# Performance work log

Hardware: AMD Instinct MI355X
Metric: run time of the kernel (lower is better)

## Reference

```python
import jax, jax.numpy as jnp
import numpy as np

EPS_COS = 1e-8   # torch CosineSimilarity default eps
EP = 0.001       # module's self.ep


def _cosine_sim(a, b):
    # torch.nn.CosineSimilarity(dim=1): dot / max(||a||*||b||, eps)
    dot = jnp.sum(a * b, axis=1)
    na = jnp.sqrt(jnp.sum(a * a, axis=1))
    nb = jnp.sqrt(jnp.sum(b * b, axis=1))
    return dot / jnp.maximum(na * nb, EPS_COS)


def setup_inputs() -> dict:
    key = jax.random.key(0)
    k1, k2, k3, k4 = jax.random.split(key, 4)
    B, D = 4096, 1024
    return {
        "question_embeddings_pos": jax.random.normal(k1, (2 * B, D), dtype=jnp.float32),
        "question_embeddings_neg": jax.random.normal(k2, (23 * B, D), dtype=jnp.float32),
        "pos_image_embeddings": jax.random.normal(k3, (2 * B, D), dtype=jnp.float32),
        "neg_image_embeddings": jax.random.normal(k4, (23 * B, D), dtype=jnp.float32),
        "batch_size": B,
    }


def reference(question_embeddings_pos, question_embeddings_neg,
              pos_image_embeddings, neg_image_embeddings, batch_size):
    epos = jnp.exp(_cosine_sim(question_embeddings_pos, pos_image_embeddings))  # [2B]
    eneg = jnp.exp(_cosine_sim(question_embeddings_neg, neg_image_embeddings))  # [23B]
    # segmented sums: groups of 2 positives and 23 negatives per batch item
    pos_sum = jnp.sum(epos.reshape(batch_size, 2), axis=1)    # [B]
    neg_sum = jnp.sum(eneg.reshape(batch_size, 23), axis=1)   # [B]
    per_item = (neg_sum - pos_sum) / (pos_sum + neg_sum + EP)
    return jnp.sum(per_item)
```

## Files before the change

### kernel.cpp

```cpp
#include <hip/hip_runtime.h>
#include <math.h>

#define D 1024
#define EPS_COS 1e-8f
#define EP 0.001f

__global__ __launch_bounds__(256) void row_cosexp_kernel(
    const float* __restrict__ qpos, const float* __restrict__ ipos,
    const float* __restrict__ qneg, const float* __restrict__ ineg,
    float* __restrict__ e, int n_pos, int n_total)
{
    const int row  = (int)((blockIdx.x * blockDim.x + threadIdx.x) >> 6);
    const int lane = threadIdx.x & 63;
    if (row >= n_total) return;

    const float* a;
    const float* b;
    if (row < n_pos) {
        a = qpos + (size_t)row * D;
        b = ipos + (size_t)row * D;
    } else {
        const size_t rn = (size_t)(row - n_pos);
        a = qneg + rn * D;
        b = ineg + rn * D;
    }
    const float4* a4 = (const float4*)a;
    const float4* b4 = (const float4*)b;

    float dab = 0.f, daa = 0.f, dbb = 0.f;
#pragma unroll
    for (int j = 0; j < 4; ++j) {
        const float4 av = a4[lane + 64 * j];
        const float4 bv = b4[lane + 64 * j];
        dab += av.x * bv.x + av.y * bv.y + av.z * bv.z + av.w * bv.w;
        daa += av.x * av.x + av.y * av.y + av.z * av.z + av.w * av.w;
        dbb += bv.x * bv.x + bv.y * bv.y + bv.z * bv.z + bv.w * bv.w;
    }

#pragma unroll
    for (int off = 32; off > 0; off >>= 1) {
        dab += __shfl_down(dab, off, 64);
        daa += __shfl_down(daa, off, 64);
        dbb += __shfl_down(dbb, off, 64);
    }

    if (lane == 0) {
        const float denom = fmaxf(sqrtf(daa) * sqrtf(dbb), EPS_COS);
        e[row] = __expf(dab / denom);
    }
}

__global__ __launch_bounds__(256) void combine_kernel(
    const float* __restrict__ e, float* __restrict__ out, int B, int n_pos)
{
    const int i = (int)(blockIdx.x * blockDim.x + threadIdx.x);
    float v = 0.f;
    if (i < B) {
        const float ps = e[2 * i] + e[2 * i + 1];
        const float* en = e + n_pos + 23 * (size_t)i;
        float ns = 0.f;
#pragma unroll
        for (int j = 0; j < 23; ++j) ns += en[j];
        v = (ns - ps) / (ps + ns + EP);
    }

#pragma unroll
    for (int off = 32; off > 0; off >>= 1) v += __shfl_down(v, off, 64);

    __shared__ float s[4];
    const int lane = threadIdx.x & 63;
    const int w    = threadIdx.x >> 6;
    if (lane == 0) s[w] = v;
    __syncthreads();
    if (threadIdx.x == 0) {
        const float t = s[0] + s[1] + s[2] + s[3];
        atomicAdd(out, t);
    }
}

extern "C" void kernel_launch(void* const* d_in, const int* in_sizes, int n_in,
                              void* d_out, int out_size, void* d_ws, size_t ws_size,
                              hipStream_t stream) {
    const float* qpos = (const float*)d_in[0];
    const float* qneg = (const float*)d_in[1];
    const float* ipos = (const float*)d_in[2];
    const float* ineg = (const float*)d_in[3];

    const int B       = in_sizes[0] / (2 * D);
    const int n_pos   = 2 * B;
    const int n_neg   = 23 * B;
    const int n_total = n_pos + n_neg;

    float* e = (float*)d_ws;

    hipMemsetAsync(d_out, 0, sizeof(float), stream);

    const int rows_per_block = 256 / 64;
    const int grid1 = (n_total + rows_per_block - 1) / rows_per_block;
    row_cosexp_kernel<<<grid1, 256, 0, stream>>>(qpos, ipos, qneg, ineg, e, n_pos, n_total);

    const int grid2 = (B + 255) / 256;
    combine_kernel<<<grid2, 256, 0, stream>>>(e, (float*)d_out, B, n_pos);
}
```

Baseline: 739.4 us.

## Fuse row cosine-exp and per-item combine into one block-per-item kernel

```diff
diff --git a/kernel.cpp b/kernel.cpp
--- a/kernel.cpp
+++ b/kernel.cpp
@@ -5,76 +5,67 @@
 #define EPS_COS 1e-8f
 #define EP 0.001f
 
-__global__ __launch_bounds__(256) void row_cosexp_kernel(
+typedef float f32x4 __attribute__((ext_vector_type(4)));
+
+__global__ __launch_bounds__(320) void fused_item_kernel(
     const float* __restrict__ qpos, const float* __restrict__ ipos,
     const float* __restrict__ qneg, const float* __restrict__ ineg,
-    float* __restrict__ e, int n_pos, int n_total)
+    float* __restrict__ out)
 {
-    const int row  = (int)((blockIdx.x * blockDim.x + threadIdx.x) >> 6);
-    const int lane = threadIdx.x & 63;
-    if (row >= n_total) return;
+    const int item = (int)blockIdx.x;
+    const int wave = (int)(threadIdx.x >> 6);
+    const int lane = (int)(threadIdx.x & 63);
 
-    const float* a;
-    const float* b;
-    if (row < n_pos) {
-        a = qpos + (size_t)row * D;
-        b = ipos + (size_t)row * D;
-    } else {
-        const size_t rn = (size_t)(row - n_pos);
-        a = qneg + rn * D;
-        b = ineg + rn * D;
-    }
-    const float4* a4 = (const float4*)a;
-    const float4* b4 = (const float4*)b;
+    float psum = 0.f, nsum = 0.f;
 
-    float dab = 0.f, daa = 0.f, dbb = 0.f;
 #pragma unroll
-    for (int j = 0; j < 4; ++j) {
-        const float4 av = a4[lane + 64 * j];
-        const float4 bv = b4[lane + 64 * j];
-        dab += av.x * bv.x + av.y * bv.y + av.z * bv.z + av.w * bv.w;
-        daa += av.x * av.x + av.y * av.y + av.z * av.z + av.w * av.w;
-        dbb += bv.x * bv.x + bv.y * bv.y + bv.z * bv.z + bv.w * bv.w;
+    for (int rr = 0; rr < 5; ++rr) {
+        const int r = wave + 5 * rr;
+        const float* a;
+        const float* b;
+        if (r < 2) {
+            const size_t off = ((size_t)(2 * item + r)) * D;
+            a = qpos + off;
+            b = ipos + off;
+        } else {
+            const size_t off = ((size_t)(23 * item + (r - 2))) * D;
+            a = qneg + off;
+            b = ineg + off;
+        }
+        const f32x4* a4 = (const f32x4*)a + lane;
+        const f32x4* b4 = (const f32x4*)b + lane;
+
+        float dab = 0.f, daa = 0.f, dbb = 0.f;
+#pragma unroll
+        for (int j = 0; j < 4; ++j) {
+            const f32x4 av = __builtin_nontemporal_load(&a4[64 * j]);
+            const f32x4 bv = __builtin_nontemporal_load(&b4[64 * j]);
+            dab += av.x * bv.x + av.y * bv.y + av.z * bv.z + av.w * bv.w;
+            daa += av.x * av.x + av.y * av.y + av.z * av.z + av.w * av.w;
+            dbb += bv.x * bv.x + bv.y * bv.y + bv.z * bv.z + bv.w * bv.w;
+        }
+
+#pragma unroll
+        for (int off = 32; off > 0; off >>= 1) {
+            dab += __shfl_down(dab, off, 64);
+            daa += __shfl_down(daa, off, 64);
+            dbb += __shfl_down(dbb, off, 64);
+        }
+
+        if (lane == 0) {
+            const float denom = fmaxf(sqrtf(daa) * sqrtf(dbb), EPS_COS);
+            const float ecs = __expf(dab / denom);
+            if (r < 2) psum += ecs; else nsum += ecs;
+        }
     }
 
-#pragma unroll
-    for (int off = 32; off > 0; off >>= 1) {
-        dab += __shfl_down(dab, off, 64);
-        daa += __shfl_down(daa, off, 64);
-        dbb += __shfl_down(dbb, off, 64);
-    }
-
-    if (lane == 0) {
-        const float denom = fmaxf(sqrtf(daa) * sqrtf(dbb), EPS_COS);
-        e[row] = __expf(dab / denom);
-    }
-}
-
-__global__ __launch_bounds__(256) void combine_kernel(
-    const float* __restrict__ e, float* __restrict__ out, int B, int n_pos)
-{
-    const int i = (int)(blockIdx.x * blockDim.x + threadIdx.x);
-    float v = 0.f;
-    if (i < B) {
-        const float ps = e[2 * i] + e[2 * i + 1];
-        const float* en = e + n_pos + 23 * (size_t)i;
-        float ns = 0.f;
-#pragma unroll
-        for (int j = 0; j < 23; ++j) ns += en[j];
-        v = (ns - ps) / (ps + ns + EP);
-    }
-
-#pragma unroll
-    for (int off = 32; off > 0; off >>= 1) v += __shfl_down(v, off, 64);
-
-    __shared__ float s[4];
-    const int lane = threadIdx.x & 63;
-    const int w    = threadIdx.x >> 6;
-    if (lane == 0) s[w] = v;
+    __shared__ float sp[5], sn[5];
+    if (lane == 0) { sp[wave] = psum; sn[wave] = nsum; }
     __syncthreads();
     if (threadIdx.x == 0) {
-        const float t = s[0] + s[1] + s[2] + s[3];
-        atomicAdd(out, t);
+        const float ps = sp[0] + sp[1] + sp[2] + sp[3] + sp[4];
+        const float ns = sn[0] + sn[1] + sn[2] + sn[3] + sn[4];
+        atomicAdd(out, (ns - ps) / (ps + ns + EP));
     }
 }
 
@@ -86,19 +77,9 @@
     const float* ipos = (const float*)d_in[2];
     const float* ineg = (const float*)d_in[3];
 
-    const int B       = in_sizes[0] / (2 * D);
-    const int n_pos   = 2 * B;
-    const int n_neg   = 23 * B;
-    const int n_total = n_pos + n_neg;
-
-    float* e = (float*)d_ws;
+    const int B = in_sizes[0] / (2 * D);
 
     hipMemsetAsync(d_out, 0, sizeof(float), stream);
 
-    const int rows_per_block = 256 / 64;
-    const int grid1 = (n_total + rows_per_block - 1) / rows_per_block;
-    row_cosexp_kernel<<<grid1, 256, 0, stream>>>(qpos, ipos, qneg, ineg, e, n_pos, n_total);
-
-    const int grid2 = (B + 255) / 256;
-    combine_kernel<<<grid2, 256, 0, stream>>>(e, (float*)d_out, B, n_pos);
+    fused_item_kernel<<<B, 320, 0, stream>>>(qpos, ipos, qneg, ineg, (float*)d_out);
 }
```

After: 713.1 us. 3.6% less time.
